# Performance work log

Measured on AMD Instinct MI355X. Metric: run time of the kernel, lower is better.

Reference implementation:

```python
import jax, jax.numpy as jnp
import numpy as np

B, GH, GW = 8, 32, 32
S = GH * GW            # 1024
HIDDEN = 512
D = 64                 # head_dim
NUM_HOPS = 2
EPS = 1e-6


def setup_inputs() -> dict:
    key = jax.random.key(0)
    ks = jax.random.split(key, 8)

    def init(k, shape, std):
        return (jax.random.normal(k, shape) * std).astype(jnp.float32)

    x = jax.random.normal(ks[0], (B, S, HIDDEN), dtype=jnp.float32)
    Wq = init(ks[1], (D, HIDDEN), HIDDEN ** -0.5)
    Wk = init(ks[2], (D, HIDDEN), HIDDEN ** -0.5)
    Wv = init(ks[3], (D, HIDDEN), HIDDEN ** -0.5)
    bias_table = init(ks[4], (2 * GH - 1, 2 * GW - 1), 0.02)
    fusion_w = jnp.ones((NUM_HOPS, 3), dtype=jnp.float32)
    fusion_b = jnp.zeros((NUM_HOPS,), dtype=jnp.float32)
    hop_W = init(ks[5], (NUM_HOPS, D, D), D ** -0.5)
    gate_W = init(ks[6], (NUM_HOPS, HIDDEN), HIDDEN ** -0.5)
    gate_b = jnp.zeros((NUM_HOPS,), dtype=jnp.float32)
    out_W = init(ks[7], (HIDDEN, D), D ** -0.5)
    temperature = jnp.ones((1,), dtype=jnp.float32)

    # relative position index [S, S] (buffer, constant)
    coords = np.stack(np.meshgrid(np.arange(GH), np.arange(GW), indexing='ij')).reshape(2, -1)
    rel = coords[:, :, None] - coords[:, None, :]
    rel[0] += GH - 1
    rel[1] += GW - 1
    rel_idx = jnp.asarray(rel[0] * (2 * GW - 1) + rel[1], dtype=jnp.int32)

    return dict(x=x, Wq=Wq, Wk=Wk, Wv=Wv, bias_table=bias_table,
                fusion_w=fusion_w, fusion_b=fusion_b, hop_W=hop_W,
                gate_W=gate_W, gate_b=gate_b, out_W=out_W,
                temperature=temperature, rel_idx=rel_idx)


def _rotate_half(u):
    d = u.shape[-1] // 2
    return jnp.concatenate([-u[..., d:], u[..., :d]], axis=-1)


def _prob_log(p):
    p = jnp.clip(p, EPS, 1.0 - EPS)
    return jnp.log(p / (1.0 - p + EPS))


def _mat_exp(M, h):
    R = M
    for _ in range(h - 1):
        R = jnp.matmul(R, M)
    return R


def _row_norm(M):
    return M / (jnp.sum(M, axis=-1, keepdims=True) + EPS)


def reference(x, Wq, Wk, Wv, bias_table, fusion_w, fusion_b, hop_W,
              gate_W, gate_b, out_W, temperature, rel_idx):
    b, s, hdim = x.shape
    d = Wq.shape[0]
    n_hops = hop_W.shape[0]
    scale = jnp.sqrt(jnp.float32(d))

    Q = jnp.einsum('bsh,dh->bsd', x, Wq)
    K = jnp.einsum('bsh,dh->bsd', x, Wk)
    V = jnp.einsum('bsh,dh->bsd', x, Wv)

    # RoPE (cached cos/sin are deterministic functions of S, D)
    inv_freq = 1.0 / (10000.0 ** (jnp.arange(0, d, 2, dtype=jnp.float32) / d))
    t = jnp.arange(s, dtype=jnp.float32)
    emb = jnp.concatenate([jnp.outer(t, inv_freq)] * 2, axis=-1)  # [S, D]
    cos, sin = jnp.cos(emb), jnp.sin(emb)
    Q = Q * cos + _rotate_half(Q) * sin
    K = K * cos + _rotate_half(K) * sin

    pb = bias_table.reshape(-1)[rel_idx]  # [S, S]
    scores = (jnp.einsum('bsd,btd->bst', Q, K) / scale + pb[None])
    scores = scores / jnp.clip(temperature, 0.1, None)
    A = jax.nn.softmax(scores, axis=-1)  # [B, S, S]

    A_T = jnp.swapaxes(A, -1, -2)
    AAt = jnp.matmul(A, A_T)
    AtA = jnp.matmul(A_T, A)

    hop_outs = []
    for hop in range(n_hops):
        h = hop + 1
        A_seq = _row_norm(_mat_exp(A, h))
        A_co = _row_norm(_mat_exp(AAt, h))
        A_sp = _row_norm(_mat_exp(AtA, h))
        fused_logit = (fusion_b[hop]
                       + fusion_w[hop, 0] * _prob_log(A_seq)
                       + fusion_w[hop, 1] * _prob_log(A_co)
                       + fusion_w[hop, 2] * _prob_log(A_sp))
        fused = _row_norm(jax.nn.sigmoid(fused_logit))
        hop_v = jnp.einsum('bsd,ed->bse', V, hop_W[hop])
        hop_outs.append(jnp.matmul(fused, hop_v))  # [B, S, D]

    gate = jax.nn.softmax(jnp.einsum('bsh,gh->bsg', x, gate_W) + gate_b, axis=-1)
    combined = sum(hop_outs[i] * gate[..., i:i + 1] for i in range(n_hops))
    return jnp.einsum('bsd,hd->bsh', combined, out_W)
```

## Files before the change

kernel.cpp:

```cpp
#include <hip/hip_runtime.h>
#include <hip/hip_bf16.h>

#define BB 8
#define SS 1024
#define HH 512
#define DD 64

typedef unsigned short u16;
typedef short v8s __attribute__((ext_vector_type(8)));
typedef float v4f __attribute__((ext_vector_type(4)));

__device__ __forceinline__ float bf2f(u16 u) {
    union { unsigned int i; float f; } v; v.i = ((unsigned int)u) << 16; return v.f;
}
__device__ __forceinline__ u16 f2bf(float f) {
    union { float f; unsigned int i; } v; v.f = f;
    unsigned int u = v.i;
    unsigned int r = u + 0x7fffu + ((u >> 16) & 1u);
    return (u16)(r >> 16);
}

__device__ __forceinline__ void gload16(const u16* g, u16* l) {
    __builtin_amdgcn_global_load_lds(
        (const __attribute__((address_space(1))) void*)g,
        (__attribute__((address_space(3))) void*)l,
        16, 0, 0);
}


__device__ __forceinline__ void tile_1024(
    const u16* __restrict__ Xb, const u16* __restrict__ Yb,
    u16* __restrict__ Cd, int tm, int tn, u16* Xs, u16* Ys)
{
    int t = threadIdx.x, lane = t & 63, w = t >> 6;
    int wm = (w & 1) << 6, wn = (w >> 1) << 6;
    int fr = lane & 15, q = lane >> 4, m7 = fr & 7;
    int subrow = lane >> 3, cch = (lane & 7) ^ subrow;

    const u16* xg[4]; const u16* yg[4]; u16* xl[4]; u16* yl[4];
    #pragma unroll
    for (int i = 0; i < 4; i++) {
        int r = i * 32 + w * 8 + subrow;
        xg[i] = Xb + (long)(tm + r) * 1024 + cch * 8;
        yg[i] = Yb + (long)(tn + r) * 1024 + cch * 8;
        xl[i] = Xs + (i * 32 + w * 8) * 64;
        yl[i] = Ys + (i * 32 + w * 8) * 64;
    }

    v4f acc[4][4];
    #pragma unroll
    for (int i = 0; i < 4; i++)
        #pragma unroll
        for (int j = 0; j < 4; j++) {
            acc[i][j][0] = 0.f; acc[i][j][1] = 0.f; acc[i][j][2] = 0.f; acc[i][j][3] = 0.f;
        }

    for (int k0 = 0; k0 < 1024; k0 += 64) {
        __syncthreads();
        #pragma unroll
        for (int i = 0; i < 4; i++) { gload16(xg[i] + k0, xl[i]); gload16(yg[i] + k0, yl[i]); }
        __syncthreads();
        v8s af[2][4], bfr[2][4];
        #pragma unroll
        for (int h = 0; h < 2; h++) {
            int ca = (((h << 2) + q) ^ m7) << 3;
            #pragma unroll
            for (int s = 0; s < 4; s++) {
                af[h][s]  = *(const v8s*)(Xs + (wm + s * 16 + fr) * 64 + ca);
                bfr[h][s] = *(const v8s*)(Ys + (wn + s * 16 + fr) * 64 + ca);
            }
        }
        #pragma unroll
        for (int h = 0; h < 2; h++)
            #pragma unroll
            for (int i = 0; i < 4; i++)
                #pragma unroll
                for (int j = 0; j < 4; j++)
                    acc[i][j] = __builtin_amdgcn_mfma_f32_16x16x32_bf16(af[h][i], bfr[h][j], acc[i][j], 0, 0, 0);
    }
    #pragma unroll
    for (int i = 0; i < 4; i++) {
        int rowb = tm + wm + i * 16 + q * 4;
        #pragma unroll
        for (int j = 0; j < 4; j++) {
            int col = tn + wn + j * 16 + fr;
            #pragma unroll
            for (int r = 0; r < 4; r++)
                Cd[(long)(rowb + r) * 1024 + col] = f2bf(acc[i][j][r]);
        }
    }
}

__device__ __forceinline__ void tile_k64(
    const u16* __restrict__ Xrows, const u16* __restrict__ Yrows,
    void* __restrict__ Cd, int crs, int cf32, u16* Xs, u16* Ys)
{
    int t = threadIdx.x, lane = t & 63, w = t >> 6;
    int wm = (w & 1) << 6, wn = (w >> 1) << 6;
    int fr = lane & 15, q = lane >> 4, m7 = fr & 7;
    int subrow = lane >> 3, cch = (lane & 7) ^ subrow;

    #pragma unroll
    for (int i = 0; i < 4; i++) {
        int r = i * 32 + w * 8 + subrow;
        gload16(Xrows + (long)r * 64 + cch * 8, Xs + (i * 32 + w * 8) * 64);
        gload16(Yrows + (long)r * 64 + cch * 8, Ys + (i * 32 + w * 8) * 64);
    }
    __syncthreads();

    v4f acc[4][4];
    #pragma unroll
    for (int i = 0; i < 4; i++)
        #pragma unroll
        for (int j = 0; j < 4; j++) {
            acc[i][j][0] = 0.f; acc[i][j][1] = 0.f; acc[i][j][2] = 0.f; acc[i][j][3] = 0.f;
        }
    v8s af[2][4], bfr[2][4];
    #pragma unroll
    for (int h = 0; h < 2; h++) {
        int ca = (((h << 2) + q) ^ m7) << 3;
        #pragma unroll
        for (int s = 0; s < 4; s++) {
            af[h][s]  = *(const v8s*)(Xs + (wm + s * 16 + fr) * 64 + ca);
            bfr[h][s] = *(const v8s*)(Ys + (wn + s * 16 + fr) * 64 + ca);
        }
    }
    #pragma unroll
    for (int h = 0; h < 2; h++)
        #pragma unroll
        for (int i = 0; i < 4; i++)
            #pragma unroll
            for (int j = 0; j < 4; j++)
                acc[i][j] = __builtin_amdgcn_mfma_f32_16x16x32_bf16(af[h][i], bfr[h][j], acc[i][j], 0, 0, 0);
    #pragma unroll
    for (int i = 0; i < 4; i++) {
        int rowb = wm + i * 16 + q * 4;
        #pragma unroll
        for (int j = 0; j < 4; j++) {
            int col = wn + j * 16 + fr;
            #pragma unroll
            for (int r = 0; r < 4; r++) {
                long o = (long)(rowb + r) * crs + col;
                if (cf32) ((float*)Cd)[o] = acc[i][j][r];
                else      ((u16*)Cd)[o] = f2bf(acc[i][j][r]);
            }
        }
    }
}

__device__ __forceinline__ void hop_tile(
    const u16* __restrict__ Fb, const u16* __restrict__ Hb,
    int y, int tmt, float* __restrict__ Pd, u16* Fs, u16* Hs)
{
    int tm = tmt * 128, kb = y * 256;
    int t = threadIdx.x, lane = t & 63, w = t >> 6;
    int fr = lane & 15, q = lane >> 4, m7 = fr & 7;
    int subrow = lane >> 3, cch = (lane & 7) ^ subrow;

    const u16* fg[4]; u16* fl[4]; const u16* hg[2]; u16* hl[2];
    #pragma unroll
    for (int i = 0; i < 4; i++) {
        int r = i * 32 + w * 8 + subrow;
        fg[i] = Fb + (long)(tm + r) * 1024 + cch * 8;
        fl[i] = Fs + (i * 32 + w * 8) * 64;
    }
    #pragma unroll
    for (int i = 0; i < 2; i++) {
        int r = i * 32 + w * 8 + subrow;
        hg[i] = Hb + (long)r * 1024 + cch * 8;
        hl[i] = Hs + (i * 32 + w * 8) * 64;
    }

    v4f acc[2][4];
    #pragma unroll
    for (int i = 0; i < 2; i++)
        #pragma unroll
        for (int j = 0; j < 4; j++) {
            acc[i][j][0] = 0.f; acc[i][j][1] = 0.f; acc[i][j][2] = 0.f; acc[i][j][3] = 0.f;
        }

    for (int k0 = kb; k0 < kb + 256; k0 += 64) {
        __syncthreads();
        #pragma unroll
        for (int i = 0; i < 4; i++) gload16(fg[i] + k0, fl[i]);
        #pragma unroll
        for (int i = 0; i < 2; i++) gload16(hg[i] + k0, hl[i]);
        __syncthreads();
        v8s af[2][2], bfr[2][4];
        #pragma unroll
        for (int h = 0; h < 2; h++) {
            int ca = (((h << 2) + q) ^ m7) << 3;
            #pragma unroll
            for (int s = 0; s < 2; s++)
                af[h][s] = *(const v8s*)(Fs + (w * 32 + s * 16 + fr) * 64 + ca);
            #pragma unroll
            for (int s = 0; s < 4; s++)
                bfr[h][s] = *(const v8s*)(Hs + (s * 16 + fr) * 64 + ca);
        }
        #pragma unroll
        for (int h = 0; h < 2; h++)
            #pragma unroll
            for (int i = 0; i < 2; i++)
                #pragma unroll
                for (int j = 0; j < 4; j++)
                    acc[i][j] = __builtin_amdgcn_mfma_f32_16x16x32_bf16(af[h][i], bfr[h][j], acc[i][j], 0, 0, 0);
    }
    #pragma unroll
    for (int i = 0; i < 2; i++) {
        int rowb = tm + w * 32 + i * 16 + q * 4;
        #pragma unroll
        for (int j = 0; j < 4; j++) {
            int col = j * 16 + fr;
            #pragma unroll
            for (int r = 0; r < 4; r++)
                Pd[(long)(rowb + r) * 64 + col] = acc[i][j][r];
        }
    }
}

__device__ __forceinline__ void mirror_tile(u16* __restrict__ C, int ti, int tj, u16* sm)
{
    int t = threadIdx.x;
    int r = t >> 1, ch = (t & 1) << 6;
    const u16* src = C + (long)(ti * 128 + r) * 1024 + tj * 128 + ch;
    #pragma unroll
    for (int p = 0; p < 8; p++) {
        uint4 v = *(const uint4*)(src + p * 8);
        *(uint4*)(&sm[r * 136 + ch + p * 8]) = v;
    }
    __syncthreads();
    u16* dst = C + (long)(tj * 128 + r) * 1024 + ti * 128 + ch;
    #pragma unroll
    for (int p = 0; p < 8; p++) {
        uint4 ov; u16* po = (u16*)&ov;
        #pragma unroll
        for (int e = 0; e < 8; e++) po[e] = sm[(ch + p * 8 + e) * 136 + r];
        *(uint4*)(dst + p * 8) = ov;
    }
}

__device__ __forceinline__ void fused_row(
    const u16* __restrict__ r1, const u16* __restrict__ r2, const u16* __restrict__ r3,
    float w0, float w1, float w2, float b0, u16* __restrict__ Frow, int lane)
{
    float m1[16], m2[16], m3[16];
    float s1 = 0.f, s2 = 0.f, s3 = 0.f;
    #pragma unroll
    for (int c = 0; c < 16; c++) {
        int j = c * 64 + lane;
        m1[c] = bf2f(r1[j]); m2[c] = bf2f(r2[j]); m3[c] = bf2f(r3[j]);
        s1 += m1[c]; s2 += m2[c]; s3 += m3[c];
    }
    #pragma unroll
    for (int o = 1; o < 64; o <<= 1) {
        s1 += __shfl_xor(s1, o); s2 += __shfl_xor(s2, o); s3 += __shfl_xor(s3, o);
    }
    float i1 = 1.f / (s1 + 1e-6f), i2 = 1.f / (s2 + 1e-6f), i3 = 1.f / (s3 + 1e-6f);
    float sig[16];
    float ssum = 0.f;
    #pragma unroll
    for (int c = 0; c < 16; c++) {
        float p1 = fminf(fmaxf(m1[c] * i1, 1e-6f), 1.0f - 1e-6f);
        float p2 = fminf(fmaxf(m2[c] * i2, 1e-6f), 1.0f - 1e-6f);
        float p3 = fminf(fmaxf(m3[c] * i3, 1e-6f), 1.0f - 1e-6f);
        float l1 = __logf(p1 / (1.0f - p1 + 1e-6f));
        float l2 = __logf(p2 / (1.0f - p2 + 1e-6f));
        float l3 = __logf(p3 / (1.0f - p3 + 1e-6f));
        float lg = b0 + w0 * l1 + w1 * l2 + w2 * l3;
        float sg = 1.0f / (1.0f + __expf(-lg));
        sig[c] = sg; ssum += sg;
    }
    #pragma unroll
    for (int o = 1; o < 64; o <<= 1) ssum += __shfl_xor(ssum, o);
    float inv = 1.0f / (ssum + 1e-6f);
    #pragma unroll
    for (int c = 0; c < 16; c++) Frow[c * 64 + lane] = f2bf(sig[c] * inv);
}

__global__ __launch_bounds__(256) void gemm_link1(
    const u16* __restrict__ A, const u16* __restrict__ AT,
    u16* __restrict__ AAt, u16* __restrict__ AtA, u16* __restrict__ A2)
{
    __shared__ u16 Xs[128 * 64];
    __shared__ u16 Ys[128 * 64];
    const long SSq = (long)SS * SS;
    int b = blockIdx.x & 7;
    int job = blockIdx.x >> 3;
    const u16* Xb; const u16* Yb; u16* Cd;
    int ti, tj;
    if (job < 72) {
        int tt = job < 36 ? job : job - 36;
        ti = 0;
        while (tt >= 8 - ti) { tt -= 8 - ti; ti++; }
        tj = ti + tt;
        if (job < 36) { Xb = A  + b * SSq; Yb = Xb; Cd = AAt + b * SSq; }
        else          { Xb = AT + b * SSq; Yb = Xb; Cd = AtA + b * SSq; }
    } else {
        int jj = job - 72;
        ti = jj >> 3; tj = jj & 7;
        Xb = A + b * SSq; Yb = AT + b * SSq; Cd = A2 + b * SSq;
    }
    tile_1024(Xb, Yb, Cd, ti * 128, tj * 128, Xs, Ys);
}

__global__ __launch_bounds__(256) void k_g2f0(
    const u16* __restrict__ AAt, const u16* __restrict__ AtA,
    u16* __restrict__ AAt2, u16* __restrict__ AtA2,
    const u16* __restrict__ A, const float* __restrict__ fw,
    const float* __restrict__ fbv, u16* __restrict__ F0)
{
    __shared__ u16 Xs[128 * 64];
    __shared__ u16 Ys[128 * 64];
    const long SSq = (long)SS * SS;
    int bx = blockIdx.x;
    if (bx < 576) {
        int z = bx & 15;
        int tt = bx >> 4, ti = 0;
        while (tt >= 8 - ti) { tt -= 8 - ti; ti++; }
        int tj = ti + tt;
        const u16* Xb = (z < 8 ? AAt : AtA) + (long)(z & 7) * SSq;
        u16* Cd = (z < 8 ? AAt2 : AtA2) + (long)(z & 7) * SSq;
        tile_1024(Xb, Xb, Cd, ti * 128, tj * 128, Xs, Ys);
    } else {
        int f = bx - 576;
        int lane = threadIdx.x & 63, w = threadIdx.x >> 6;
        float w0 = fw[0], w1 = fw[1], w2 = fw[2], b0 = fbv[0];
        long row = (long)f * 4 + w;
        fused_row(A + row * 1024, AAt + row * 1024, AtA + row * 1024,
                  w0, w1, w2, b0, F0 + row * 1024, lane);
    }
}

__global__ __launch_bounds__(256) void k_m2h0(
    u16* __restrict__ AAt2, u16* __restrict__ AtA2,
    const u16* __restrict__ F0, const u16* __restrict__ hopVT,
    float* __restrict__ Pa, float* __restrict__ Pb)
{
    __shared__ __align__(16) u16 sm[128 * 136];
    const long SSq = (long)SS * SS;
    int bx = blockIdx.x;
    if (bx < 448) {
        int z = bx & 15;
        int tt = bx >> 4, ti = 0;
        while (tt >= 7 - ti) { tt -= 7 - ti; ti++; }
        int tj = ti + 1 + tt;
        u16* C = (z < 8 ? AAt2 : AtA2) + (long)(z & 7) * SSq;
        mirror_tile(C, ti, tj, sm);
    } else {
        int j = bx - 448;
        int y = j >> 6, rest = j & 63;
        int tmt = rest >> 3, b = rest & 7;
        float* Pd = (y < 2 ? Pa + (long)y * 16 * 65536 : Pb + (long)(y - 2) * 16 * 65536)
                    + (long)b * 65536;
        hop_tile(F0 + (long)b * SSq, hopVT + (long)b * 65536, y, tmt, Pd,
                 sm, sm + 128 * 64);
    }
}

__global__ __launch_bounds__(256) void gemm_hop1(
    const u16* __restrict__ F1, const u16* __restrict__ hopVT,
    float* __restrict__ Pa, float* __restrict__ Pb)
{
    __shared__ u16 Fs[128 * 64];
    __shared__ u16 Hs[64 * 64];
    const long SSq = (long)SS * SS;
    int j = blockIdx.x;
    int y = j >> 6, rest = j & 63;
    int tmt = rest >> 3, b = rest & 7;
    float* Pd = (y < 2 ? Pa + (long)y * 16 * 65536 : Pb + (long)(y - 2) * 16 * 65536)
                + (long)(8 + b) * 65536;
    hop_tile(F1 + (long)b * SSq, hopVT + (long)(8 + b) * 65536, y, tmt, Pd, Fs, Hs);
}

__global__ __launch_bounds__(256) void gemm_nt(
    const u16* __restrict__ X, long sx,
    const u16* __restrict__ Y, long sy,
    void* __restrict__ Cv, long sc,
    int M, int N, int K, int cf32)
{
    __shared__ u16 Xs[128 * 64];
    __shared__ u16 Ys[128 * 64];
    const u16* Xb = X + (long)blockIdx.z * sx;
    const u16* Yb = Y + (long)blockIdx.z * sy;
    int tm = blockIdx.x * 128, tn = blockIdx.y * 128;
    int t = threadIdx.x, lane = t & 63, w = t >> 6;
    int wm = (w & 1) << 6, wn = (w >> 1) << 6;
    int fr = lane & 15, q = lane >> 4, m7 = fr & 7;
    int subrow = lane >> 3, cch = (lane & 7) ^ subrow;

    const u16* xg[4]; const u16* yg[4]; u16* xl[4]; u16* yl[4];
    #pragma unroll
    for (int i = 0; i < 4; i++) {
        int r = i * 32 + w * 8 + subrow;
        xg[i] = Xb + (long)(tm + r) * K + cch * 8;
        yg[i] = Yb + (long)(tn + r) * K + cch * 8;
        xl[i] = Xs + (i * 32 + w * 8) * 64;
        yl[i] = Ys + (i * 32 + w * 8) * 64;
    }

    v4f acc[4][4];
    #pragma unroll
    for (int i = 0; i < 4; i++)
        #pragma unroll
        for (int j = 0; j < 4; j++) {
            acc[i][j][0] = 0.f; acc[i][j][1] = 0.f; acc[i][j][2] = 0.f; acc[i][j][3] = 0.f;
        }

    for (int k0 = 0; k0 < K; k0 += 64) {
        __syncthreads();
        #pragma unroll
        for (int i = 0; i < 4; i++) { gload16(xg[i] + k0, xl[i]); gload16(yg[i] + k0, yl[i]); }
        __syncthreads();
        v8s af[2][4], bfr[2][4];
        #pragma unroll
        for (int h = 0; h < 2; h++) {
            int ca = (((h << 2) + q) ^ m7) << 3;
            #pragma unroll
            for (int s = 0; s < 4; s++) {
                af[h][s]  = *(const v8s*)(Xs + (wm + s * 16 + fr) * 64 + ca);
                bfr[h][s] = *(const v8s*)(Ys + (wn + s * 16 + fr) * 64 + ca);
            }
        }
        #pragma unroll
        for (int h = 0; h < 2; h++)
            #pragma unroll
            for (int i = 0; i < 4; i++)
                #pragma unroll
                for (int j = 0; j < 4; j++)
                    acc[i][j] = __builtin_amdgcn_mfma_f32_16x16x32_bf16(af[h][i], bfr[h][j], acc[i][j], 0, 0, 0);
    }
    long cb = (long)blockIdx.z * sc;
    #pragma unroll
    for (int i = 0; i < 4; i++) {
        int rowb = tm + wm + i * 16 + q * 4;
        #pragma unroll
        for (int j = 0; j < 4; j++) {
            int col = tn + wn + j * 16 + fr;
            #pragma unroll
            for (int r = 0; r < 4; r++) {
                long o = cb + (long)(rowb + r) * N + col;
                if (cf32) ((float*)Cv)[o] = acc[i][j][r];
                else      ((u16*)Cv)[o] = f2bf(acc[i][j][r]);
            }
        }
    }
}

__global__ __launch_bounds__(256) void k_qk_hopv(
    const u16* __restrict__ Qb, const u16* __restrict__ Kb,
    const u16* __restrict__ Vb, const u16* __restrict__ hopWb,
    float* __restrict__ scores, u16* __restrict__ hopvC)
{
    __shared__ u16 Xs[128 * 64];
    __shared__ u16 Ys[128 * 64];
    const long SSq = (long)SS * SS;
    const long SD = (long)SS * DD;
    int bx = blockIdx.x;
    if (bx < 512) {
        int z = bx & 7;
        int tt = bx >> 3;
        int tm = (tt >> 3) * 128, tn = (tt & 7) * 128;
        tile_k64(Qb + z * SD + (long)tm * 64, Kb + z * SD + (long)tn * 64,
                 scores + z * SSq + (long)tm * 1024 + tn, 1024, 1, Xs, Ys);
    } else {
        int tm = (bx - 512) * 128;
        tile_k64(Vb + (long)tm * 64, hopWb,
                 hopvC + (long)tm * 128, 128, 0, Xs, Ys);
    }
}

__global__ __launch_bounds__(256) void k_sm_hvt(
    const float* __restrict__ scores, const float* __restrict__ btab,
    const float* __restrict__ temp, u16* __restrict__ A,
    const u16* __restrict__ hopvC, u16* __restrict__ hopVT)
{
    __shared__ __align__(16) float smf[3969];
    int bx = blockIdx.x;
    int t = threadIdx.x;
    if (bx < 2048) {
        for (int i = t; i < 3969; i += 256) smf[i] = btab[i];
        __syncthreads();
        int lane = t & 63, w = t >> 6;
        long row = (long)bx * 4 + w;
        int i = (int)(row & 1023);
        int ih = i >> 5, iw = i & 31;
        float inv_t = 1.0f / fmaxf(temp[0], 0.1f);
        const float* srow = scores + row * 1024;
        float sc[16];
        float m = -1e30f;
        #pragma unroll
        for (int c = 0; c < 16; c++) {
            int j = c * 64 + lane;
            int jh = j >> 5, jw = j & 31;
            float pb = smf[(ih - jh + 31) * 63 + (iw - jw + 31)];
            float s = (srow[j] * 0.125f + pb) * inv_t;
            sc[c] = s; m = fmaxf(m, s);
        }
        #pragma unroll
        for (int o = 1; o < 64; o <<= 1) m = fmaxf(m, __shfl_xor(m, o));
        float sum = 0.f;
        #pragma unroll
        for (int c = 0; c < 16; c++) { sc[c] = __expf(sc[c] - m); sum += sc[c]; }
        #pragma unroll
        for (int o = 1; o < 64; o <<= 1) sum += __shfl_xor(sum, o);
        float inv = 1.0f / sum;
        #pragma unroll
        for (int c = 0; c < 16; c++) A[row * 1024 + c * 64 + lane] = f2bf(sc[c] * inv);
    } else {
        u16* tile = (u16*)smf;
        int ex = bx - 2048;
        int hop = ex >> 7, rem = ex & 127;
        int z = rem & 7, i0 = (rem >> 3) * 64;
        const u16* s = hopvC + (long)z * (1024 * 128) + hop * 64;
        u16* d = hopVT + (long)(hop * 8 + z) * 65536;
        int r = t >> 2, c0 = (t & 3) << 4;
        #pragma unroll
        for (int p = 0; p < 2; p++) {
            int c = c0 + p * 8;
            uint4 v = *(const uint4*)(s + (long)(i0 + r) * 128 + c);
            *(uint4*)(&tile[r * 72 + c]) = v;
        }
        __syncthreads();
        #pragma unroll
        for (int p = 0; p < 2; p++) {
            uint4 ov; u16* po = (u16*)&ov;
            #pragma unroll
            for (int e = 0; e < 8; e++) po[e] = tile[(c0 + p * 8 + e) * 72 + r];
            *(uint4*)(d + (long)r * 1024 + i0 + c0 + p * 8) = ov;
        }
    }
}

__global__ __launch_bounds__(256) void k_mirror(u16* __restrict__ C0, u16* __restrict__ C1)
{
    __shared__ __align__(16) u16 sm[128 * 136];
    const long SSq = (long)SS * SS;
    int z = blockIdx.z;
    u16* C = (z < 8 ? C0 : C1) + (long)(z & 7) * SSq;
    int tt = blockIdx.x, ti = 0;
    while (tt >= 7 - ti) { tt -= 7 - ti; ti++; }
    int tj = ti + 1 + tt;
    mirror_tile(C, ti, tj, sm);
}

__global__ __launch_bounds__(256) void k_fused1(
    const u16* __restrict__ A2, const u16* __restrict__ AAt2,
    const u16* __restrict__ AtA2, const float* __restrict__ fw,
    const float* __restrict__ fbv, u16* __restrict__ F1)
{
    int lane = threadIdx.x & 63, w = threadIdx.x >> 6;
    float w0 = fw[3], w1 = fw[4], w2 = fw[5], b0 = fbv[1];
    long row = (long)blockIdx.x * 4 + w;
    fused_row(A2 + row * 1024, AAt2 + row * 1024, AtA2 + row * 1024,
              w0, w1, w2, b0, F1 + row * 1024, lane);
}

__global__ __launch_bounds__(256) void k_pack(
    const float* __restrict__ x, const float* __restrict__ Wq,
    const float* __restrict__ Wk, const float* __restrict__ Wv,
    const float* __restrict__ gW, const float* __restrict__ hopW,
    const float* __restrict__ outW, u16* __restrict__ xb,
    u16* __restrict__ wpack, u16* __restrict__ hopWb, u16* __restrict__ outWb)
{
    int bx = blockIdx.x;
    if (bx < 4096) {
        long i = (long)bx * 256 + threadIdx.x;
        float4 v = ((const float4*)x)[i];
        ushort4 o;
        o.x = f2bf(v.x); o.y = f2bf(v.y); o.z = f2bf(v.z); o.w = f2bf(v.w);
        ((ushort4*)xb)[i] = o;
    } else {
        int idx = (bx - 4096) * 256 + threadIdx.x;
        if (idx < 131072) {
            int r = idx >> 9, c = idx & 511;
            float v = 0.f;
            if (r < 64)       v = Wq[r * 512 + c];
            else if (r < 128) v = Wk[(r - 64) * 512 + c];
            else if (r < 192) v = Wv[(r - 128) * 512 + c];
            else if (r < 194) v = gW[(r - 192) * 512 + c];
            wpack[idx] = f2bf(v);
        } else if (idx < 131072 + 8192) {
            int i = idx - 131072;
            hopWb[i] = f2bf(hopW[i]);
        } else if (idx < 131072 + 8192 + 32768) {
            int i = idx - 131072 - 8192;
            outWb[i] = f2bf(outW[i]);
        }
    }
}

__global__ __launch_bounds__(256) void k_rope(
    const float* __restrict__ QKVG, const float* __restrict__ gateb,
    u16* __restrict__ Qb, u16* __restrict__ Kb, u16* __restrict__ Vb,
    float* __restrict__ gate)
{
    int t = threadIdx.x, l = t & 63, w = t >> 6;
    long row = (long)blockIdx.x * 4 + w;
    int spos = (int)(row & (SS - 1));
    const float* base = QKVG + row * 256;
    float q = base[l], k = base[64 + l], v = base[128 + l];
    float qp = __shfl_xor(q, 32), kp = __shfl_xor(k, 32);
    float sgn = (l < 32) ? -1.f : 1.f;
    int f = l & 31;
    float ang = (float)spos * exp2f(-(float)f * (13.287712379549449f / 32.0f));
    float cs = cosf(ang), sn = sinf(ang);
    Qb[row * 64 + l] = f2bf(q * cs + sgn * qp * sn);
    Kb[row * 64 + l] = f2bf(k * cs + sgn * kp * sn);
    Vb[row * 64 + l] = f2bf(v);
    if (l < 2) {
        float g0 = base[192] + gateb[0], g1 = base[193] + gateb[1];
        float m = fmaxf(g0, g1);
        float e0 = __expf(g0 - m), e1 = __expf(g1 - m);
        gate[row * 2 + l] = ((l == 0) ? e0 : e1) / (e0 + e1);
    }
}

__global__ __launch_bounds__(256) void k_transpose(
    const u16* __restrict__ src, u16* __restrict__ dst,
    int srs, int drs, long sbs, long dbs)
{
    __shared__ u16 tile[64 * 72];
    const u16* s = src + (long)blockIdx.z * sbs;
    u16* d = dst + (long)blockIdx.z * dbs;
    int i0 = blockIdx.x * 64, j0 = blockIdx.y * 64;
    int t = threadIdx.x;
    int r = t >> 2, c0 = (t & 3) << 4;
    #pragma unroll
    for (int p = 0; p < 2; p++) {
        int c = c0 + p * 8;
        uint4 v = *(const uint4*)(s + (long)(i0 + r) * srs + j0 + c);
        *(uint4*)(&tile[r * 72 + c]) = v;
    }
    __syncthreads();
    #pragma unroll
    for (int p = 0; p < 2; p++) {
        uint4 ov;
        u16* po = (u16*)&ov;
        #pragma unroll
        for (int e = 0; e < 8; e++) po[e] = tile[(c0 + p * 8 + e) * 72 + r];
        *(uint4*)(d + (long)(j0 + r) * drs + i0 + c0 + p * 8) = ov;
    }
}

__global__ __launch_bounds__(256) void k_combine(
    const float* __restrict__ Pa, const float* __restrict__ Pb,
    const float* __restrict__ gate, u16* __restrict__ comb)
{
    long idx = (long)blockIdx.x * 256 + threadIdx.x;
    long srow = idx >> 6;
    int b = (int)(srow >> 10);
    long o = (long)(srow & 1023) * 64 + (idx & 63);
    float h0 = Pa[(long)b * 65536 + o] + Pa[(long)(16 + b) * 65536 + o]
             + Pb[(long)b * 65536 + o] + Pb[(long)(16 + b) * 65536 + o];
    float h1 = Pa[(long)(8 + b) * 65536 + o] + Pa[(long)(24 + b) * 65536 + o]
             + Pb[(long)(8 + b) * 65536 + o] + Pb[(long)(24 + b) * 65536 + o];
    float g0 = gate[srow * 2], g1 = gate[srow * 2 + 1];
    comb[idx] = f2bf(h0 * g0 + h1 * g1);
}

extern "C" void kernel_launch(void* const* d_in, const int* in_sizes, int n_in,
                              void* d_out, int out_size, void* d_ws, size_t ws_size,
                              hipStream_t stream) {
    const float* x    = (const float*)d_in[0];
    const float* Wq   = (const float*)d_in[1];
    const float* Wk   = (const float*)d_in[2];
    const float* Wv   = (const float*)d_in[3];
    const float* btab = (const float*)d_in[4];
    const float* fw   = (const float*)d_in[5];
    const float* fbv  = (const float*)d_in[6];
    const float* hopW = (const float*)d_in[7];
    const float* gW   = (const float*)d_in[8];
    const float* gb   = (const float*)d_in[9];
    const float* outW = (const float*)d_in[10];
    const float* temp = (const float*)d_in[11];
    float* out = (float*)d_out;

    char* wsb = (char*)d_ws;
    size_t off = 0;
    auto take = [&](size_t n) { char* p = wsb + off; off += (n + 255) & ~(size_t)255; return p; };
    u16* Qb      = (u16*)take(8192L * 64 * 2);
    u16* Kb      = (u16*)take(8192L * 64 * 2);
    u16* Vb      = (u16*)take(8192L * 64 * 2);
    float* gate  = (float*)take(8192L * 2 * 4);
    u16* wpack   = (u16*)take(256L * 512 * 2);
    u16* hopWb   = (u16*)take(2L * 64 * 64 * 2);
    u16* outWb   = (u16*)take(512L * 64 * 2);
    u16* hopvC   = (u16*)take(8192L * 128 * 2);
    u16* hopVT   = (u16*)take(2L * 8 * 64 * 1024 * 2);
    float* Pa    = (float*)take(2L * 16 * 65536 * 4);
    u16* comb    = (u16*)take(8192L * 64 * 2);
    float* scoresF = (float*)take(8L * 1024 * 1024 * 4);
    float* QKVG  = (float*)scoresF;
    u16* F0      = (u16*)scoresF;
    u16* F1      = (u16*)scoresF + 8L * 1024 * 1024;
    u16* A       = (u16*)take(8L * 1024 * 1024 * 2);
    u16* xb      = (u16*)A;
    u16* AT      = (u16*)take(8L * 1024 * 1024 * 2);
    float* Pb    = (float*)AT;
    u16* AAt     = (u16*)take(8L * 1024 * 1024 * 2);
    u16* AtA     = (u16*)take(8L * 1024 * 1024 * 2);
    u16* A2      = (u16*)take(8L * 1024 * 1024 * 2);
    u16* AAt2    = (u16*)take(8L * 1024 * 1024 * 2);
    u16* AtA2    = (u16*)take(8L * 1024 * 1024 * 2);
    (void)ws_size; (void)in_sizes; (void)n_in; (void)out_size;

    const long SSq = (long)SS * SS;

    k_pack<<<4768, 256, 0, stream>>>(x, Wq, Wk, Wv, gW, hopW, outW, xb, wpack, hopWb, outWb);
    gemm_nt<<<dim3(64, 2, 1), 256, 0, stream>>>(xb, 0, wpack, 0, QKVG, 0, 8192, 256, 512, 1);
    k_rope<<<2048, 256, 0, stream>>>(QKVG, gb, Qb, Kb, Vb, gate);
    k_qk_hopv<<<576, 256, 0, stream>>>(Qb, Kb, Vb, hopWb, scoresF, hopvC);
    k_sm_hvt<<<2304, 256, 0, stream>>>(scoresF, btab, temp, A, hopvC, hopVT);
    k_transpose<<<dim3(16, 16, 8), 256, 0, stream>>>(A, AT, 1024, 1024, SSq, SSq);
    gemm_link1<<<1088, 256, 0, stream>>>(A, AT, AAt, AtA, A2);
    k_mirror<<<dim3(28, 1, 16), 256, 0, stream>>>(AAt, AtA);
    k_g2f0<<<2624, 256, 0, stream>>>(AAt, AtA, AAt2, AtA2, A, fw, fbv, F0);
    k_m2h0<<<704, 256, 0, stream>>>(AAt2, AtA2, F0, hopVT, Pa, Pb);
    k_fused1<<<2048, 256, 0, stream>>>(A2, AAt2, AtA2, fw, fbv, F1);
    gemm_hop1<<<256, 256, 0, stream>>>(F1, hopVT, Pa, Pb);
    k_combine<<<2048, 256, 0, stream>>>(Pa, Pb, gate, comb);
    gemm_nt<<<dim3(64, 4, 1), 256, 0, stream>>>(comb, 0, outWb, 0, out, 0, 8192, 512, 64, 1);
}
```

Measured before the change: 321.0 us.

## Fuse symmetric-tile mirroring into GEMM epilogue and regroup fused/hop kernels

The symmetric GEMMs (AAt, AtA and their squares) now write the transposed copy of each off-diagonal tile straight from registers through shared memory in the GEMM epilogue. This removes the separate k_mirror pass and the mirror phase of k_m2h0, which each re-read tiles from global memory. The fused-probability computation for hop 0 becomes its own kernel, k_fused0, and the hop-0 output tiles now run in the same launch as the second-level GEMM. That cuts the launch count and global traffic, at the cost of extra barriers and shared-memory transpose work inside GEMM blocks.

Measured after the change: 333.8 us. +4.0%, slower.

```diff
diff --git a/kernel.cpp b/kernel.cpp
--- a/kernel.cpp
+++ b/kernel.cpp
@@ -27,10 +27,9 @@
         16, 0, 0);
 }
 
-
 __device__ __forceinline__ void tile_1024(
     const u16* __restrict__ Xb, const u16* __restrict__ Yb,
-    u16* __restrict__ Cd, int tm, int tn, u16* Xs, u16* Ys)
+    u16* __restrict__ Cd, int tm, int tn, u16* Xs, u16* Ys, int mirror)
 {
     int t = threadIdx.x, lane = t & 63, w = t >> 6;
     int wm = (w & 1) << 6, wn = (w >> 1) << 6;
@@ -89,6 +88,33 @@
                 Cd[(long)(rowb + r) * 1024 + col] = f2bf(acc[i][j][r]);
         }
     }
+    if (mirror) {
+        u16* sm2 = Xs;
+        #pragma unroll
+        for (int p = 0; p < 2; p++) {
+            __syncthreads();
+            if ((w & 1) == p) {
+                #pragma unroll
+                for (int i = 0; i < 4; i++)
+                    #pragma unroll
+                    for (int j = 0; j < 4; j++) {
+                        int col = wn + j * 16 + fr;
+                        #pragma unroll
+                        for (int r = 0; r < 4; r++)
+                            sm2[(i * 16 + q * 4 + r) * 136 + col] = f2bf(acc[i][j][r]);
+                    }
+            }
+            __syncthreads();
+            int rr = t >> 1, h2 = t & 1;
+            #pragma unroll
+            for (int v = 0; v < 4; v++) {
+                uint4 ov; u16* po = (u16*)&ov;
+                #pragma unroll
+                for (int e = 0; e < 8; e++) po[e] = sm2[(h2 * 32 + v * 8 + e) * 136 + rr];
+                *(uint4*)(Cd + (long)(tn + rr) * 1024 + tm + p * 64 + h2 * 32 + v * 8) = ov;
+            }
+        }
+    }
 }
 
 __device__ __forceinline__ void tile_k64(
@@ -215,27 +241,6 @@
             for (int r = 0; r < 4; r++)
                 Pd[(long)(rowb + r) * 64 + col] = acc[i][j][r];
         }
-    }
-}
-
-__device__ __forceinline__ void mirror_tile(u16* __restrict__ C, int ti, int tj, u16* sm)
-{
-    int t = threadIdx.x;
-    int r = t >> 1, ch = (t & 1) << 6;
-    const u16* src = C + (long)(ti * 128 + r) * 1024 + tj * 128 + ch;
-    #pragma unroll
-    for (int p = 0; p < 8; p++) {
-        uint4 v = *(const uint4*)(src + p * 8);
-        *(uint4*)(&sm[r * 136 + ch + p * 8]) = v;
-    }
-    __syncthreads();
-    u16* dst = C + (long)(tj * 128 + r) * 1024 + ti * 128 + ch;
-    #pragma unroll
-    for (int p = 0; p < 8; p++) {
-        uint4 ov; u16* po = (u16*)&ov;
-        #pragma unroll
-        for (int e = 0; e < 8; e++) po[e] = sm[(ch + p * 8 + e) * 136 + r];
-        *(uint4*)(dst + p * 8) = ov;
     }
 }
 
@@ -281,36 +286,36 @@
     const u16* __restrict__ A, const u16* __restrict__ AT,
     u16* __restrict__ AAt, u16* __restrict__ AtA, u16* __restrict__ A2)
 {
-    __shared__ u16 Xs[128 * 64];
-    __shared__ u16 Ys[128 * 64];
+    __shared__ __align__(16) u16 sm[16384];
+    u16* Xs = sm; u16* Ys = sm + 8192;
     const long SSq = (long)SS * SS;
     int b = blockIdx.x & 7;
     int job = blockIdx.x >> 3;
     const u16* Xb; const u16* Yb; u16* Cd;
-    int ti, tj;
+    int ti, tj, mir;
     if (job < 72) {
         int tt = job < 36 ? job : job - 36;
         ti = 0;
         while (tt >= 8 - ti) { tt -= 8 - ti; ti++; }
         tj = ti + tt;
+        mir = (ti != tj);
         if (job < 36) { Xb = A  + b * SSq; Yb = Xb; Cd = AAt + b * SSq; }
         else          { Xb = AT + b * SSq; Yb = Xb; Cd = AtA + b * SSq; }
     } else {
         int jj = job - 72;
-        ti = jj >> 3; tj = jj & 7;
+        ti = jj >> 3; tj = jj & 7; mir = 0;
         Xb = A + b * SSq; Yb = AT + b * SSq; Cd = A2 + b * SSq;
     }
-    tile_1024(Xb, Yb, Cd, ti * 128, tj * 128, Xs, Ys);
-}
-
-__global__ __launch_bounds__(256) void k_g2f0(
+    tile_1024(Xb, Yb, Cd, ti * 128, tj * 128, Xs, Ys, mir);
+}
+
+__global__ __launch_bounds__(256) void gemm_link2h0(
     const u16* __restrict__ AAt, const u16* __restrict__ AtA,
     u16* __restrict__ AAt2, u16* __restrict__ AtA2,
-    const u16* __restrict__ A, const float* __restrict__ fw,
-    const float* __restrict__ fbv, u16* __restrict__ F0)
-{
-    __shared__ u16 Xs[128 * 64];
-    __shared__ u16 Ys[128 * 64];
+    const u16* __restrict__ F0, const u16* __restrict__ hopVT,
+    float* __restrict__ Pa, float* __restrict__ Pb)
+{
+    __shared__ __align__(16) u16 sm[16384];
     const long SSq = (long)SS * SS;
     int bx = blockIdx.x;
     if (bx < 576) {
@@ -320,40 +325,15 @@
         int tj = ti + tt;
         const u16* Xb = (z < 8 ? AAt : AtA) + (long)(z & 7) * SSq;
         u16* Cd = (z < 8 ? AAt2 : AtA2) + (long)(z & 7) * SSq;
-        tile_1024(Xb, Xb, Cd, ti * 128, tj * 128, Xs, Ys);
+        tile_1024(Xb, Xb, Cd, ti * 128, tj * 128, sm, sm + 8192, ti != tj);
     } else {
-        int f = bx - 576;
-        int lane = threadIdx.x & 63, w = threadIdx.x >> 6;
-        float w0 = fw[0], w1 = fw[1], w2 = fw[2], b0 = fbv[0];
-        long row = (long)f * 4 + w;
-        fused_row(A + row * 1024, AAt + row * 1024, AtA + row * 1024,
-                  w0, w1, w2, b0, F0 + row * 1024, lane);
-    }
-}
-
-__global__ __launch_bounds__(256) void k_m2h0(
-    u16* __restrict__ AAt2, u16* __restrict__ AtA2,
-    const u16* __restrict__ F0, const u16* __restrict__ hopVT,
-    float* __restrict__ Pa, float* __restrict__ Pb)
-{
-    __shared__ __align__(16) u16 sm[128 * 136];
-    const long SSq = (long)SS * SS;
-    int bx = blockIdx.x;
-    if (bx < 448) {
-        int z = bx & 15;
-        int tt = bx >> 4, ti = 0;
-        while (tt >= 7 - ti) { tt -= 7 - ti; ti++; }
-        int tj = ti + 1 + tt;
-        u16* C = (z < 8 ? AAt2 : AtA2) + (long)(z & 7) * SSq;
-        mirror_tile(C, ti, tj, sm);
-    } else {
-        int j = bx - 448;
+        int j = bx - 576;
         int y = j >> 6, rest = j & 63;
         int tmt = rest >> 3, b = rest & 7;
         float* Pd = (y < 2 ? Pa + (long)y * 16 * 65536 : Pb + (long)(y - 2) * 16 * 65536)
                     + (long)b * 65536;
         hop_tile(F0 + (long)b * SSq, hopVT + (long)b * 65536, y, tmt, Pd,
-                 sm, sm + 128 * 64);
+                 sm, sm + 8192);
     }
 }
 
@@ -531,16 +511,16 @@
     }
 }
 
-__global__ __launch_bounds__(256) void k_mirror(u16* __restrict__ C0, u16* __restrict__ C1)
-{
-    __shared__ __align__(16) u16 sm[128 * 136];
-    const long SSq = (long)SS * SS;
-    int z = blockIdx.z;
-    u16* C = (z < 8 ? C0 : C1) + (long)(z & 7) * SSq;
-    int tt = blockIdx.x, ti = 0;
-    while (tt >= 7 - ti) { tt -= 7 - ti; ti++; }
-    int tj = ti + 1 + tt;
-    mirror_tile(C, ti, tj, sm);
+__global__ __launch_bounds__(256) void k_fused0(
+    const u16* __restrict__ A, const u16* __restrict__ AAt,
+    const u16* __restrict__ AtA, const float* __restrict__ fw,
+    const float* __restrict__ fbv, u16* __restrict__ F0)
+{
+    int lane = threadIdx.x & 63, w = threadIdx.x >> 6;
+    float w0 = fw[0], w1 = fw[1], w2 = fw[2], b0 = fbv[0];
+    long row = (long)blockIdx.x * 4 + w;
+    fused_row(A + row * 1024, AAt + row * 1024, AtA + row * 1024,
+              w0, w1, w2, b0, F0 + row * 1024, lane);
 }
 
 __global__ __launch_bounds__(256) void k_fused1(
@@ -713,9 +693,8 @@
     k_sm_hvt<<<2304, 256, 0, stream>>>(scoresF, btab, temp, A, hopvC, hopVT);
     k_transpose<<<dim3(16, 16, 8), 256, 0, stream>>>(A, AT, 1024, 1024, SSq, SSq);
     gemm_link1<<<1088, 256, 0, stream>>>(A, AT, AAt, AtA, A2);
-    k_mirror<<<dim3(28, 1, 16), 256, 0, stream>>>(AAt, AtA);
-    k_g2f0<<<2624, 256, 0, stream>>>(AAt, AtA, AAt2, AtA2, A, fw, fbv, F0);
-    k_m2h0<<<704, 256, 0, stream>>>(AAt2, AtA2, F0, hopVT, Pa, Pb);
+    k_fused0<<<2048, 256, 0, stream>>>(A, AAt, AtA, fw, fbv, F0);
+    gemm_link2h0<<<832, 256, 0, stream>>>(AAt, AtA, AAt2, AtA2, F0, hopVT, Pa, Pb);
     k_fused1<<<2048, 256, 0, stream>>>(A2, AAt2, AtA2, fw, fbv, F1);
     gemm_hop1<<<256, 256, 0, stream>>>(F1, hopVT, Pa, Pb);
     k_combine<<<2048, 256, 0, stream>>>(Pa, Pb, gate, comb);
```

## Vectorize fused_row loads and regroup hop-0 work across kernels

Applied to the files above, without the earlier changes.

fused_row now reads 16 contiguous bf16 values per lane as two 16-byte loads and writes its output the same way, replacing strided scalar accesses. The hop-0 fused-row pass moves into its own kernel that runs before a combined kernel doing the AAt2/AtA2 GEMM tiles and the hop-0 hop_tile GEMMs. The mirror of AAt2/AtA2 then runs as a separate kernel. This reshuffles which work shares a launch to improve load balance and memory access width, at the cost of one extra launch and less overlap between the fused pass and the GEMMs.

Result: no change. 327.3 us (+1.9%).

```diff
diff --git a/kernel.cpp b/kernel.cpp
--- a/kernel.cpp
+++ b/kernel.cpp
@@ -243,14 +243,22 @@
     const u16* __restrict__ r1, const u16* __restrict__ r2, const u16* __restrict__ r3,
     float w0, float w1, float w2, float b0, u16* __restrict__ Frow, int lane)
 {
+    int base = lane << 4;
+    union U { uint4 v; u16 s[8]; };
+    U a[2], b[2], c[2];
+    a[0].v = *(const uint4*)(r1 + base); a[1].v = *(const uint4*)(r1 + base + 8);
+    b[0].v = *(const uint4*)(r2 + base); b[1].v = *(const uint4*)(r2 + base + 8);
+    c[0].v = *(const uint4*)(r3 + base); c[1].v = *(const uint4*)(r3 + base + 8);
     float m1[16], m2[16], m3[16];
     float s1 = 0.f, s2 = 0.f, s3 = 0.f;
     #pragma unroll
-    for (int c = 0; c < 16; c++) {
-        int j = c * 64 + lane;
-        m1[c] = bf2f(r1[j]); m2[c] = bf2f(r2[j]); m3[c] = bf2f(r3[j]);
-        s1 += m1[c]; s2 += m2[c]; s3 += m3[c];
-    }
+    for (int h = 0; h < 2; h++)
+        #pragma unroll
+        for (int e = 0; e < 8; e++) {
+            int k = h * 8 + e;
+            m1[k] = bf2f(a[h].s[e]); m2[k] = bf2f(b[h].s[e]); m3[k] = bf2f(c[h].s[e]);
+            s1 += m1[k]; s2 += m2[k]; s3 += m3[k];
+        }
     #pragma unroll
     for (int o = 1; o < 64; o <<= 1) {
         s1 += __shfl_xor(s1, o); s2 += __shfl_xor(s2, o); s3 += __shfl_xor(s3, o);
@@ -259,22 +267,25 @@
     float sig[16];
     float ssum = 0.f;
     #pragma unroll
-    for (int c = 0; c < 16; c++) {
-        float p1 = fminf(fmaxf(m1[c] * i1, 1e-6f), 1.0f - 1e-6f);
-        float p2 = fminf(fmaxf(m2[c] * i2, 1e-6f), 1.0f - 1e-6f);
-        float p3 = fminf(fmaxf(m3[c] * i3, 1e-6f), 1.0f - 1e-6f);
+    for (int k = 0; k < 16; k++) {
+        float p1 = fminf(fmaxf(m1[k] * i1, 1e-6f), 1.0f - 1e-6f);
+        float p2 = fminf(fmaxf(m2[k] * i2, 1e-6f), 1.0f - 1e-6f);
+        float p3 = fminf(fmaxf(m3[k] * i3, 1e-6f), 1.0f - 1e-6f);
         float l1 = __logf(p1 / (1.0f - p1 + 1e-6f));
         float l2 = __logf(p2 / (1.0f - p2 + 1e-6f));
         float l3 = __logf(p3 / (1.0f - p3 + 1e-6f));
         float lg = b0 + w0 * l1 + w1 * l2 + w2 * l3;
         float sg = 1.0f / (1.0f + __expf(-lg));
-        sig[c] = sg; ssum += sg;
+        sig[k] = sg; ssum += sg;
     }
     #pragma unroll
     for (int o = 1; o < 64; o <<= 1) ssum += __shfl_xor(ssum, o);
     float inv = 1.0f / (ssum + 1e-6f);
-    #pragma unroll
-    for (int c = 0; c < 16; c++) Frow[c * 64 + lane] = f2bf(sig[c] * inv);
+    U o0, o1;
+    #pragma unroll
+    for (int e = 0; e < 8; e++) { o0.s[e] = f2bf(sig[e] * inv); o1.s[e] = f2bf(sig[8 + e] * inv); }
+    *(uint4*)(Frow + base) = o0.v;
+    *(uint4*)(Frow + base + 8) = o1.v;
 }
 
 __global__ __launch_bounds__(256) void gemm_link1(
@@ -303,11 +314,11 @@
     tile_1024(Xb, Yb, Cd, ti * 128, tj * 128, Xs, Ys);
 }
 
-__global__ __launch_bounds__(256) void k_g2f0(
+__global__ __launch_bounds__(256) void gemm_link2h0(
     const u16* __restrict__ AAt, const u16* __restrict__ AtA,
     u16* __restrict__ AAt2, u16* __restrict__ AtA2,
-    const u16* __restrict__ A, const float* __restrict__ fw,
-    const float* __restrict__ fbv, u16* __restrict__ F0)
+    const u16* __restrict__ F0, const u16* __restrict__ hopVT,
+    float* __restrict__ Pa, float* __restrict__ Pb)
 {
     __shared__ u16 Xs[128 * 64];
     __shared__ u16 Ys[128 * 64];
@@ -322,38 +333,12 @@
         u16* Cd = (z < 8 ? AAt2 : AtA2) + (long)(z & 7) * SSq;
         tile_1024(Xb, Xb, Cd, ti * 128, tj * 128, Xs, Ys);
     } else {
-        int f = bx - 576;
-        int lane = threadIdx.x & 63, w = threadIdx.x >> 6;
-        float w0 = fw[0], w1 = fw[1], w2 = fw[2], b0 = fbv[0];
-        long row = (long)f * 4 + w;
-        fused_row(A + row * 1024, AAt + row * 1024, AtA + row * 1024,
-                  w0, w1, w2, b0, F0 + row * 1024, lane);
-    }
-}
-
-__global__ __launch_bounds__(256) void k_m2h0(
-    u16* __restrict__ AAt2, u16* __restrict__ AtA2,
-    const u16* __restrict__ F0, const u16* __restrict__ hopVT,
-    float* __restrict__ Pa, float* __restrict__ Pb)
-{
-    __shared__ __align__(16) u16 sm[128 * 136];
-    const long SSq = (long)SS * SS;
-    int bx = blockIdx.x;
-    if (bx < 448) {
-        int z = bx & 15;
-        int tt = bx >> 4, ti = 0;
-        while (tt >= 7 - ti) { tt -= 7 - ti; ti++; }
-        int tj = ti + 1 + tt;
-        u16* C = (z < 8 ? AAt2 : AtA2) + (long)(z & 7) * SSq;
-        mirror_tile(C, ti, tj, sm);
-    } else {
-        int j = bx - 448;
+        int j = bx - 576;
         int y = j >> 6, rest = j & 63;
         int tmt = rest >> 3, b = rest & 7;
         float* Pd = (y < 2 ? Pa + (long)y * 16 * 65536 : Pb + (long)(y - 2) * 16 * 65536)
                     + (long)b * 65536;
-        hop_tile(F0 + (long)b * SSq, hopVT + (long)b * 65536, y, tmt, Pd,
-                 sm, sm + 128 * 64);
+        hop_tile(F0 + (long)b * SSq, hopVT + (long)b * 65536, y, tmt, Pd, Xs, Ys);
     }
 }
 
@@ -541,6 +526,18 @@
     while (tt >= 7 - ti) { tt -= 7 - ti; ti++; }
     int tj = ti + 1 + tt;
     mirror_tile(C, ti, tj, sm);
+}
+
+__global__ __launch_bounds__(256) void k_fused0(
+    const u16* __restrict__ A, const u16* __restrict__ AAt,
+    const u16* __restrict__ AtA, const float* __restrict__ fw,
+    const float* __restrict__ fbv, u16* __restrict__ F0)
+{
+    int lane = threadIdx.x & 63, w = threadIdx.x >> 6;
+    float w0 = fw[0], w1 = fw[1], w2 = fw[2], b0 = fbv[0];
+    long row = (long)blockIdx.x * 4 + w;
+    fused_row(A + row * 1024, AAt + row * 1024, AtA + row * 1024,
+              w0, w1, w2, b0, F0 + row * 1024, lane);
 }
 
 __global__ __launch_bounds__(256) void k_fused1(
@@ -714,8 +711,9 @@
     k_transpose<<<dim3(16, 16, 8), 256, 0, stream>>>(A, AT, 1024, 1024, SSq, SSq);
     gemm_link1<<<1088, 256, 0, stream>>>(A, AT, AAt, AtA, A2);
     k_mirror<<<dim3(28, 1, 16), 256, 0, stream>>>(AAt, AtA);
-    k_g2f0<<<2624, 256, 0, stream>>>(AAt, AtA, AAt2, AtA2, A, fw, fbv, F0);
-    k_m2h0<<<704, 256, 0, stream>>>(AAt2, AtA2, F0, hopVT, Pa, Pb);
+    k_fused0<<<2048, 256, 0, stream>>>(A, AAt, AtA, fw, fbv, F0);
+    gemm_link2h0<<<832, 256, 0, stream>>>(AAt, AtA, AAt2, AtA2, F0, hopVT, Pa, Pb);
+    k_mirror<<<dim3(28, 1, 16), 256, 0, stream>>>(AAt2, AtA2);
     k_fused1<<<2048, 256, 0, stream>>>(A2, AAt2, AtA2, fw, fbv, F1);
     gemm_hop1<<<256, 256, 0, stream>>>(F1, hopVT, Pa, Pb);
     k_combine<<<2048, 256, 0, stream>>>(Pa, Pb, gate, comb);
```
